# Optimization experiments

Measured on AMD Instinct MI355X. Metric: run time of the kernel, lower is better.

The kernel has to match this reference:

```python
import jax, jax.numpy as jnp
import numpy as np
import math

B, Q, CQ = 2, 2048, 512
H, D = 8, 64  # no_heads, c_hidden

def setup_inputs() -> dict:
    key = jax.random.key(0)
    ks = jax.random.split(key, 8)
    s = 0.02
    return {
        "q_x": jax.random.normal(ks[0], (B, Q, CQ), jnp.float32),
        "kv_x": jax.random.normal(ks[1], (B, Q, CQ), jnp.float32),
        "bias": jax.random.normal(ks[2], (B, 1, Q, Q), jnp.float32),
        "w_qkv": jax.random.normal(ks[3], (3 * H * D, CQ), jnp.float32) * s,
        "w_o": jax.random.normal(ks[4], (CQ, H * D), jnp.float32) * s,
        "b_o": jnp.zeros((CQ,), jnp.float32),
        "w_g": jax.random.normal(ks[5], (H * D, CQ), jnp.float32) * s,
        "b_g": jnp.zeros((H * D,), jnp.float32),
    }

def reference(q_x, kv_x, bias, w_qkv, w_o, b_o, w_g, b_g):
    # Fused QKV projection from q_x (kv_x is unused by the original module's _prep_qkv)
    qkv = jnp.einsum('bqc,ec->bqe', q_x, w_qkv)  # [B,Q,3*H*D]
    q, k, v = jnp.split(qkv, 3, axis=-1)
    q = q.reshape(B, Q, H, D) / math.sqrt(D)
    k = k.reshape(B, Q, H, D)
    v = v.reshape(B, Q, H, D)
    # scores + additive pairwise bias, softmax over keys
    scores = jnp.einsum('bqhd,bkhd->bhqk', q, k) + bias  # [B,H,Q,K]
    attn = jax.nn.softmax(scores, axis=-1)
    o = jnp.einsum('bhqk,bkhd->bqhd', attn, v)  # [B,Q,H,D]
    # sigmoid gating
    g = jax.nn.sigmoid(jnp.einsum('bqc,ec->bqe', q_x, w_g) + b_g).reshape(B, Q, H, D)
    o = o * g
    # output projection
    o = o.reshape(B, Q, H * D)
    return jnp.einsum('bqe,ce->bqc', o, w_o) + b_o
```

## Files before the change

kernel.cpp:

```cpp
#include <hip/hip_runtime.h>
#include <math.h>

#define B_  2
#define Q_  2048
#define CQ_ 512
#define H_  8
#define D_  64
#define M_  (B_*Q_)

typedef __bf16 bf16;
typedef __bf16 bf16x8 __attribute__((ext_vector_type(8)));
typedef float  f32x4  __attribute__((ext_vector_type(4)));

__device__ __forceinline__ void gl_lds16(const bf16* g, bf16* l) {
    __builtin_amdgcn_global_load_lds(
        (const __attribute__((address_space(1))) unsigned int*)g,
        (__attribute__((address_space(3))) unsigned int*)l, 16, 0, 0);
}

#define S0 (4096*512)
#define S1 (1536*512)
#define S2 (512*512)
#define S3 (512*512)
__global__ __launch_bounds__(256)
void convert_kernel(const float* __restrict__ qx, const float* __restrict__ wqkv,
                    const float* __restrict__ wg, const float* __restrict__ wo,
                    bf16* __restrict__ qxb, bf16* __restrict__ wcat, bf16* __restrict__ wob)
{
    const long long t = (long long)blockIdx.x * 256 + threadIdx.x;
    const long long e = t * 8;
    const float* src; bf16* dst;
    if (e < S0)                { src = qx + e;                  dst = qxb + e; }
    else if (e < S0 + S1)      { src = wqkv + (e - S0);         dst = wcat + (e - S0); }
    else if (e < S0 + S1 + S2) { src = wg + (e - S0 - S1);      dst = wcat + S1 + (e - S0 - S1); }
    else                       { src = wo + (e - S0 - S1 - S2); dst = wob + (e - S0 - S1 - S2); }
    const float4 a = *(const float4*)(src);
    const float4 b = *(const float4*)(src + 4);
    bf16x8 v;
    v[0] = (bf16)a.x; v[1] = (bf16)a.y; v[2] = (bf16)a.z; v[3] = (bf16)a.w;
    v[4] = (bf16)b.x; v[5] = (bf16)b.y; v[6] = (bf16)b.z; v[7] = (bf16)b.w;
    *(bf16x8*)dst = v;
}

template<int BM, int BN, int EPI>
__global__ __launch_bounds__(256)
void gemm_bf16(const bf16* __restrict__ A, const bf16* __restrict__ W,
               const float* __restrict__ bvec, float* __restrict__ fout,
               bf16* __restrict__ qb, bf16* __restrict__ kb, bf16* __restrict__ vb,
               bf16* __restrict__ gb)
{
    constexpr int MI = BM / 32, NJ = BN / 32;
    __shared__ __align__(16) bf16 As[BM * 32];
    __shared__ __align__(16) bf16 Bs[BN * 32];

    const int t = threadIdx.x;
    const int w = t >> 6, lane = t & 63;
    const int l15 = lane & 15, quad = lane >> 4;
    const int wm = w & 1, wn = w >> 1;
    const int bm = blockIdx.x * BM;
    const int bn = blockIdx.y * BN;

    f32x4 acc[MI][NJ] = {};

    const int rr = t >> 2;
    const int cc = (t & 3) * 8;

    for (int k0 = 0; k0 < 512; k0 += 32) {
        #pragma unroll
        for (int i = 0; i < BM / 64; ++i)
            gl_lds16(A + (size_t)(bm + i * 64 + rr) * 512 + k0 + cc,
                     As + (i * 64 + w * 16) * 32);
        #pragma unroll
        for (int i = 0; i < BN / 64; ++i)
            gl_lds16(W + (size_t)(bn + i * 64 + rr) * 512 + k0 + cc,
                     Bs + (i * 64 + w * 16) * 32);
        __asm__ volatile("s_waitcnt vmcnt(0)" ::: "memory");
        __syncthreads();

        bf16x8 af[MI], bfr[NJ];
        #pragma unroll
        for (int i = 0; i < MI; ++i)
            af[i] = *(const bf16x8*)(As + (wm * (BM / 2) + i * 16 + l15) * 32 + quad * 8);
        #pragma unroll
        for (int j = 0; j < NJ; ++j)
            bfr[j] = *(const bf16x8*)(Bs + (wn * (BN / 2) + j * 16 + l15) * 32 + quad * 8);
        #pragma unroll
        for (int i = 0; i < MI; ++i)
            #pragma unroll
            for (int j = 0; j < NJ; ++j)
                acc[i][j] = __builtin_amdgcn_mfma_f32_16x16x32_bf16(af[i], bfr[j], acc[i][j], 0, 0, 0);
        __syncthreads();
    }

    #pragma unroll
    for (int i = 0; i < MI; ++i) {
        #pragma unroll
        for (int r = 0; r < 4; ++r) {
            const int m = bm + wm * (BM / 2) + i * 16 + quad * 4 + r;
            const int b = m >> 11, qq = m & 2047;
            #pragma unroll
            for (int j = 0; j < NJ; ++j) {
                const int n = bn + wn * (BN / 2) + j * 16 + l15;
                const float c = acc[i][j][r];
                if constexpr (EPI == 0) {
                    const int part = n >> 9;
                    const int h = (n >> 6) & 7, d = n & 63;
                    if (part == 0)
                        qb[(((size_t)(b * H_ + h)) * Q_ + qq) * D_ + d] = (bf16)(c * 0.125f);
                    else if (part == 1)
                        kb[(((size_t)(b * H_ + h)) * Q_ + qq) * D_ + d] = (bf16)c;
                    else if (part == 2)
                        vb[(((size_t)(b * H_ + h)) * D_ + d) * Q_ + qq] = (bf16)c;
                    else {
                        const int gcol = n & 511;
                        const float x = c + bvec[gcol];
                        gb[(size_t)m * 512 + gcol] = (bf16)(1.f / (1.f + __expf(-x)));
                    }
                } else {
                    fout[(size_t)m * 512 + n] = c + bvec[n];
                }
            }
        }
    }
}

__global__ __launch_bounds__(256)
void attn_kernel(const bf16* __restrict__ qb, const bf16* __restrict__ kb,
                 const bf16* __restrict__ vb, const float* __restrict__ bias,
                 const bf16* __restrict__ g, bf16* __restrict__ og)
{
    __shared__ __align__(16) bf16 Ks[64 * 80];
    __shared__ __align__(16) bf16 Vs[64 * 80];
    __shared__ __align__(16) bf16 Ps[4][16 * 80];

    const int tid  = threadIdx.x;
    const int wv   = tid >> 6, lane = tid & 63;
    const int l15  = lane & 15, quad = lane >> 4;
    const int bh   = blockIdx.y;
    const int b    = bh >> 3, h = bh & 7;
    const int q0   = blockIdx.x * 64;
    const int qrow = q0 + wv * 16;

    const bf16* qptr = qb + ((size_t)bh * Q_ + qrow + l15) * D_;
    const bf16x8 aq0 = *(const bf16x8*)(qptr + quad * 8);
    const bf16x8 aq1 = *(const bf16x8*)(qptr + 32 + quad * 8);

    f32x4 acc_o[4] = {};
    float mrow[4] = {-INFINITY, -INFINITY, -INFINITY, -INFINITY};
    float lrow[4] = {0.f, 0.f, 0.f, 0.f};

    const bf16*  kbase = kb + (size_t)bh * Q_ * D_;
    const bf16*  vbase = vb + (size_t)bh * D_ * Q_;
    const float* brow  = bias + (size_t)b * Q_ * Q_;

    for (int k0 = 0; k0 < Q_; k0 += 64) {
        __syncthreads();
        #pragma unroll
        for (int p = 0; p < 2; ++p) {
            const int elem = p * 2048 + tid * 8;
            const int rr = elem >> 6, cc = elem & 63;
            *(float4*)(Ks + rr * 80 + cc) =
                *(const float4*)(kbase + (size_t)k0 * 64 + elem);
            *(float4*)(Vs + rr * 80 + cc) =
                *(const float4*)(vbase + (size_t)rr * Q_ + k0 + cc);
        }
        __syncthreads();

        float sc[4][4];
        #pragma unroll
        for (int kt = 0; kt < 4; ++kt) {
            f32x4 sacc = {0.f, 0.f, 0.f, 0.f};
            const bf16* kp = Ks + (kt * 16 + l15) * 80 + quad * 8;
            const bf16x8 bk0 = *(const bf16x8*)(kp);
            const bf16x8 bk1 = *(const bf16x8*)(kp + 32);
            sacc = __builtin_amdgcn_mfma_f32_16x16x32_bf16(aq0, bk0, sacc, 0, 0, 0);
            sacc = __builtin_amdgcn_mfma_f32_16x16x32_bf16(aq1, bk1, sacc, 0, 0, 0);
            const float* bp = brow + (size_t)(qrow + quad * 4) * Q_ + k0 + kt * 16 + l15;
            #pragma unroll
            for (int r = 0; r < 4; ++r) sc[kt][r] = sacc[r] + bp[(size_t)r * Q_];
        }

        float tmax[4];
        #pragma unroll
        for (int r = 0; r < 4; ++r)
            tmax[r] = fmaxf(fmaxf(sc[0][r], sc[1][r]), fmaxf(sc[2][r], sc[3][r]));
        #pragma unroll
        for (int off = 1; off < 16; off <<= 1)
            #pragma unroll
            for (int r = 0; r < 4; ++r)
                tmax[r] = fmaxf(tmax[r], __shfl_xor(tmax[r], off, 64));

        float alpha[4];
        #pragma unroll
        for (int r = 0; r < 4; ++r) {
            const float mn = fmaxf(mrow[r], tmax[r]);
            alpha[r] = __expf(mrow[r] - mn);
            mrow[r] = mn;
        }
        float rsum[4];
        #pragma unroll
        for (int r = 0; r < 4; ++r) {
            #pragma unroll
            for (int kt = 0; kt < 4; ++kt) sc[kt][r] = __expf(sc[kt][r] - mrow[r]);
            rsum[r] = sc[0][r] + sc[1][r] + sc[2][r] + sc[3][r];
        }
        #pragma unroll
        for (int off = 1; off < 16; off <<= 1)
            #pragma unroll
            for (int r = 0; r < 4; ++r)
                rsum[r] += __shfl_xor(rsum[r], off, 64);
        #pragma unroll
        for (int r = 0; r < 4; ++r) lrow[r] = lrow[r] * alpha[r] + rsum[r];
        #pragma unroll
        for (int dt = 0; dt < 4; ++dt)
            #pragma unroll
            for (int r = 0; r < 4; ++r) acc_o[dt][r] *= alpha[r];

        bf16* pw = Ps[wv];
        #pragma unroll
        for (int kt = 0; kt < 4; ++kt)
            #pragma unroll
            for (int r = 0; r < 4; ++r)
                pw[(quad * 4 + r) * 80 + kt * 16 + l15] = (bf16)sc[kt][r];
        __asm__ volatile("s_waitcnt lgkmcnt(0)" ::: "memory");

        #pragma unroll
        for (int kt2 = 0; kt2 < 2; ++kt2) {
            const bf16x8 ap = *(const bf16x8*)(pw + l15 * 80 + kt2 * 32 + quad * 8);
            #pragma unroll
            for (int dt = 0; dt < 4; ++dt) {
                const bf16x8 bv = *(const bf16x8*)(Vs + (dt * 16 + l15) * 80 + kt2 * 32 + quad * 8);
                acc_o[dt] = __builtin_amdgcn_mfma_f32_16x16x32_bf16(ap, bv, acc_o[dt], 0, 0, 0);
            }
        }
    }

    #pragma unroll
    for (int r = 0; r < 4; ++r) {
        const float inv = 1.f / lrow[r];
        const int qg = qrow + quad * 4 + r;
        const size_t rowoff = ((size_t)(b * Q_ + qg)) * 512 + h * 64;
        #pragma unroll
        for (int dt = 0; dt < 4; ++dt) {
            const int col = dt * 16 + l15;
            og[rowoff + col] = (bf16)(acc_o[dt][r] * inv * (float)g[rowoff + col]);
        }
    }
}

extern "C" void kernel_launch(void* const* d_in, const int* in_sizes, int n_in,
                              void* d_out, int out_size, void* d_ws, size_t ws_size,
                              hipStream_t stream)
{
    const float* q_x   = (const float*)d_in[0];
    const float* bias  = (const float*)d_in[2];
    const float* w_qkv = (const float*)d_in[3];
    const float* w_o   = (const float*)d_in[4];
    const float* b_o   = (const float*)d_in[5];
    const float* w_g   = (const float*)d_in[6];
    const float* b_g   = (const float*)d_in[7];
    float* out = (float*)d_out;

    char* ws = (char*)d_ws;
    bf16* qxb  = (bf16*)(ws);
    bf16* wcat = (bf16*)(ws + (4u  << 20));
    bf16* wob  = (bf16*)(ws + (6u  << 20));
    bf16* qb   = (bf16*)(ws + (8u  << 20));
    bf16* kb   = (bf16*)(ws + (12u << 20));
    bf16* vb   = (bf16*)(ws + (16u << 20));
    bf16* gb   = (bf16*)(ws + (20u << 20));
    bf16* ogb  = (bf16*)(ws + (24u << 20));

    convert_kernel<<<(S0 + S1 + S2 + S3) / (256 * 8), 256, 0, stream>>>(
        q_x, w_qkv, w_g, w_o, qxb, wcat, wob);
    gemm_bf16<128, 128, 0><<<dim3(32, 16), 256, 0, stream>>>(
        qxb, wcat, b_g, nullptr, qb, kb, vb, gb);
    attn_kernel<<<dim3(Q_ / 64, B_ * H_), 256, 0, stream>>>(qb, kb, vb, bias, gb, ogb);
    gemm_bf16<64, 128, 1><<<dim3(64, 4), 256, 0, stream>>>(
        ogb, wob, b_o, out, nullptr, nullptr, nullptr, nullptr);
}
```

Baseline: 204.2 us.

## Double-buffer K/V tiles, transpose MFMA operands, vectorize bias loads in attention

Restructures the attention kernel to compute S^T (K as the A operand, Q as B), so each lane owns one query row. Bias can then be loaded as contiguous float4 and the softmax reductions need only two cross-lane shuffles instead of four per value. K/V tiles and bias are prefetched into registers one iteration ahead into a double-buffered LDS with padding 72, which removes one barrier per iteration. The grid is also reordered so that the blocks of one query tile, which share bias rows across heads, run close together. The cost is higher register pressure from the prefetch buffers and more LDS use.

```diff
diff --git a/kernel.cpp b/kernel.cpp
--- a/kernel.cpp
+++ b/kernel.cpp
@@ -9,6 +9,7 @@
 #define M_  (B_*Q_)
 
 typedef __bf16 bf16;
+typedef __bf16 bf16x4 __attribute__((ext_vector_type(4)));
 typedef __bf16 bf16x8 __attribute__((ext_vector_type(8)));
 typedef float  f32x4  __attribute__((ext_vector_type(4)));
 
@@ -129,122 +130,147 @@
                  const bf16* __restrict__ vb, const float* __restrict__ bias,
                  const bf16* __restrict__ g, bf16* __restrict__ og)
 {
-    __shared__ __align__(16) bf16 Ks[64 * 80];
-    __shared__ __align__(16) bf16 Vs[64 * 80];
-    __shared__ __align__(16) bf16 Ps[4][16 * 80];
+    __shared__ __align__(16) bf16 Ks[2][64 * 72];
+    __shared__ __align__(16) bf16 Vs[2][64 * 72];
+    __shared__ __align__(16) bf16 Ps[4][16 * 72];
 
     const int tid  = threadIdx.x;
     const int wv   = tid >> 6, lane = tid & 63;
     const int l15  = lane & 15, quad = lane >> 4;
-    const int bh   = blockIdx.y;
+    const int bh   = blockIdx.x;
     const int b    = bh >> 3, h = bh & 7;
-    const int q0   = blockIdx.x * 64;
-    const int qrow = q0 + wv * 16;
-
-    const bf16* qptr = qb + ((size_t)bh * Q_ + qrow + l15) * D_;
-    const bf16x8 aq0 = *(const bf16x8*)(qptr + quad * 8);
-    const bf16x8 aq1 = *(const bf16x8*)(qptr + 32 + quad * 8);
-
-    f32x4 acc_o[4] = {};
-    float mrow[4] = {-INFINITY, -INFINITY, -INFINITY, -INFINITY};
-    float lrow[4] = {0.f, 0.f, 0.f, 0.f};
+    const int q0   = blockIdx.y * 64;
+    const int qrow = q0 + wv * 16 + l15;
+
+    const bf16* qptr = qb + ((size_t)bh * Q_ + qrow) * D_;
+    const bf16x8 bq0 = *(const bf16x8*)(qptr + quad * 8);
+    const bf16x8 bq1 = *(const bf16x8*)(qptr + 32 + quad * 8);
+
+    f32x4 acc[4] = {};
+    float m_run = -INFINITY, l_run = 0.f;
 
     const bf16*  kbase = kb + (size_t)bh * Q_ * D_;
     const bf16*  vbase = vb + (size_t)bh * D_ * Q_;
-    const float* brow  = bias + (size_t)b * Q_ * Q_;
-
-    for (int k0 = 0; k0 < Q_; k0 += 64) {
-        __syncthreads();
-        #pragma unroll
-        for (int p = 0; p < 2; ++p) {
-            const int elem = p * 2048 + tid * 8;
-            const int rr = elem >> 6, cc = elem & 63;
-            *(float4*)(Ks + rr * 80 + cc) =
-                *(const float4*)(kbase + (size_t)k0 * 64 + elem);
-            *(float4*)(Vs + rr * 80 + cc) =
-                *(const float4*)(vbase + (size_t)rr * Q_ + k0 + cc);
-        }
-        __syncthreads();
+    const float* brow  = bias + ((size_t)b * Q_ + qrow) * Q_;
+
+    const int sr  = tid >> 3;
+    const int sc8 = (tid & 7) * 8;
+
+    float4 kreg0, kreg1, vreg0, vreg1;
+    float4 bias_cur[4], bias_nxt[4];
+
+    kreg0 = *(const float4*)(kbase + (size_t)sr * 64 + sc8);
+    kreg1 = *(const float4*)(kbase + (size_t)(32 + sr) * 64 + sc8);
+    vreg0 = *(const float4*)(vbase + (size_t)sr * Q_ + sc8);
+    vreg1 = *(const float4*)(vbase + (size_t)(32 + sr) * Q_ + sc8);
+    #pragma unroll
+    for (int kt = 0; kt < 4; ++kt)
+        bias_cur[kt] = *(const float4*)(brow + kt * 16 + quad * 4);
+    *(float4*)(Ks[0] + sr * 72 + sc8) = kreg0;
+    *(float4*)(Ks[0] + (32 + sr) * 72 + sc8) = kreg1;
+    *(float4*)(Vs[0] + sr * 72 + sc8) = vreg0;
+    *(float4*)(Vs[0] + (32 + sr) * 72 + sc8) = vreg1;
+    __syncthreads();
+
+    int cur = 0;
+    for (int t = 0; t < 32; ++t) {
+        if (t < 31) {
+            const int k0n = (t + 1) * 64;
+            kreg0 = *(const float4*)(kbase + ((size_t)k0n + sr) * 64 + sc8);
+            kreg1 = *(const float4*)(kbase + ((size_t)k0n + 32 + sr) * 64 + sc8);
+            vreg0 = *(const float4*)(vbase + (size_t)sr * Q_ + k0n + sc8);
+            vreg1 = *(const float4*)(vbase + (size_t)(32 + sr) * Q_ + k0n + sc8);
+            #pragma unroll
+            for (int kt = 0; kt < 4; ++kt)
+                bias_nxt[kt] = *(const float4*)(brow + k0n + kt * 16 + quad * 4);
+        }
+
+        const bf16* Kc = Ks[cur];
+        const bf16* Vc = Vs[cur];
 
         float sc[4][4];
         #pragma unroll
         for (int kt = 0; kt < 4; ++kt) {
             f32x4 sacc = {0.f, 0.f, 0.f, 0.f};
-            const bf16* kp = Ks + (kt * 16 + l15) * 80 + quad * 8;
-            const bf16x8 bk0 = *(const bf16x8*)(kp);
-            const bf16x8 bk1 = *(const bf16x8*)(kp + 32);
-            sacc = __builtin_amdgcn_mfma_f32_16x16x32_bf16(aq0, bk0, sacc, 0, 0, 0);
-            sacc = __builtin_amdgcn_mfma_f32_16x16x32_bf16(aq1, bk1, sacc, 0, 0, 0);
-            const float* bp = brow + (size_t)(qrow + quad * 4) * Q_ + k0 + kt * 16 + l15;
-            #pragma unroll
-            for (int r = 0; r < 4; ++r) sc[kt][r] = sacc[r] + bp[(size_t)r * Q_];
-        }
-
-        float tmax[4];
+            const bf16* kp = Kc + (kt * 16 + l15) * 72 + quad * 8;
+            const bf16x8 ak0 = *(const bf16x8*)(kp);
+            const bf16x8 ak1 = *(const bf16x8*)(kp + 32);
+            sacc = __builtin_amdgcn_mfma_f32_16x16x32_bf16(ak0, bq0, sacc, 0, 0, 0);
+            sacc = __builtin_amdgcn_mfma_f32_16x16x32_bf16(ak1, bq1, sacc, 0, 0, 0);
+            sc[kt][0] = sacc[0] + bias_cur[kt].x;
+            sc[kt][1] = sacc[1] + bias_cur[kt].y;
+            sc[kt][2] = sacc[2] + bias_cur[kt].z;
+            sc[kt][3] = sacc[3] + bias_cur[kt].w;
+        }
+
+        float tmax = -INFINITY;
+        #pragma unroll
+        for (int kt = 0; kt < 4; ++kt)
+            tmax = fmaxf(tmax, fmaxf(fmaxf(sc[kt][0], sc[kt][1]),
+                                     fmaxf(sc[kt][2], sc[kt][3])));
+        tmax = fmaxf(tmax, __shfl_xor(tmax, 16, 64));
+        tmax = fmaxf(tmax, __shfl_xor(tmax, 32, 64));
+
+        const float mn = fmaxf(m_run, tmax);
+        const float alpha = __expf(m_run - mn);
+        m_run = mn;
+
+        float rsum = 0.f;
+        #pragma unroll
+        for (int kt = 0; kt < 4; ++kt)
+            #pragma unroll
+            for (int r = 0; r < 4; ++r) {
+                sc[kt][r] = __expf(sc[kt][r] - mn);
+                rsum += sc[kt][r];
+            }
+        rsum += __shfl_xor(rsum, 16, 64);
+        rsum += __shfl_xor(rsum, 32, 64);
+        l_run = l_run * alpha + rsum;
+        #pragma unroll
+        for (int dt = 0; dt < 4; ++dt) acc[dt] *= alpha;
+
+        bf16* pw = Ps[wv] + l15 * 72;
+        #pragma unroll
+        for (int kt = 0; kt < 4; ++kt) {
+            bf16x4 p4;
+            p4[0] = (bf16)sc[kt][0]; p4[1] = (bf16)sc[kt][1];
+            p4[2] = (bf16)sc[kt][2]; p4[3] = (bf16)sc[kt][3];
+            *(bf16x4*)(pw + kt * 16 + quad * 4) = p4;
+        }
+        __asm__ volatile("s_waitcnt lgkmcnt(0)" ::: "memory");
+
+        #pragma unroll
+        for (int kt2 = 0; kt2 < 2; ++kt2) {
+            const bf16x8 bp = *(const bf16x8*)(pw + kt2 * 32 + quad * 8);
+            #pragma unroll
+            for (int dt = 0; dt < 4; ++dt) {
+                const bf16x8 av = *(const bf16x8*)(Vc + (dt * 16 + l15) * 72 + kt2 * 32 + quad * 8);
+                acc[dt] = __builtin_amdgcn_mfma_f32_16x16x32_bf16(av, bp, acc[dt], 0, 0, 0);
+            }
+        }
+
+        if (t < 31) {
+            *(float4*)(Ks[cur ^ 1] + sr * 72 + sc8) = kreg0;
+            *(float4*)(Ks[cur ^ 1] + (32 + sr) * 72 + sc8) = kreg1;
+            *(float4*)(Vs[cur ^ 1] + sr * 72 + sc8) = vreg0;
+            *(float4*)(Vs[cur ^ 1] + (32 + sr) * 72 + sc8) = vreg1;
+            #pragma unroll
+            for (int kt = 0; kt < 4; ++kt) bias_cur[kt] = bias_nxt[kt];
+        }
+        __syncthreads();
+        cur ^= 1;
+    }
+
+    const float inv = 1.f / l_run;
+    const size_t obase = ((size_t)(b * Q_ + qrow)) * 512 + h * 64;
+    #pragma unroll
+    for (int dt = 0; dt < 4; ++dt) {
+        const bf16x4 gv = *(const bf16x4*)(g + obase + dt * 16 + quad * 4);
+        bf16x4 ov;
         #pragma unroll
         for (int r = 0; r < 4; ++r)
-            tmax[r] = fmaxf(fmaxf(sc[0][r], sc[1][r]), fmaxf(sc[2][r], sc[3][r]));
-        #pragma unroll
-        for (int off = 1; off < 16; off <<= 1)
-            #pragma unroll
-            for (int r = 0; r < 4; ++r)
-                tmax[r] = fmaxf(tmax[r], __shfl_xor(tmax[r], off, 64));
-
-        float alpha[4];
-        #pragma unroll
-        for (int r = 0; r < 4; ++r) {
-            const float mn = fmaxf(mrow[r], tmax[r]);
-            alpha[r] = __expf(mrow[r] - mn);
-            mrow[r] = mn;
-        }
-        float rsum[4];
-        #pragma unroll
-        for (int r = 0; r < 4; ++r) {
-            #pragma unroll
-            for (int kt = 0; kt < 4; ++kt) sc[kt][r] = __expf(sc[kt][r] - mrow[r]);
-            rsum[r] = sc[0][r] + sc[1][r] + sc[2][r] + sc[3][r];
-        }
-        #pragma unroll
-        for (int off = 1; off < 16; off <<= 1)
-            #pragma unroll
-            for (int r = 0; r < 4; ++r)
-                rsum[r] += __shfl_xor(rsum[r], off, 64);
-        #pragma unroll
-        for (int r = 0; r < 4; ++r) lrow[r] = lrow[r] * alpha[r] + rsum[r];
-        #pragma unroll
-        for (int dt = 0; dt < 4; ++dt)
-            #pragma unroll
-            for (int r = 0; r < 4; ++r) acc_o[dt][r] *= alpha[r];
-
-        bf16* pw = Ps[wv];
-        #pragma unroll
-        for (int kt = 0; kt < 4; ++kt)
-            #pragma unroll
-            for (int r = 0; r < 4; ++r)
-                pw[(quad * 4 + r) * 80 + kt * 16 + l15] = (bf16)sc[kt][r];
-        __asm__ volatile("s_waitcnt lgkmcnt(0)" ::: "memory");
-
-        #pragma unroll
-        for (int kt2 = 0; kt2 < 2; ++kt2) {
-            const bf16x8 ap = *(const bf16x8*)(pw + l15 * 80 + kt2 * 32 + quad * 8);
-            #pragma unroll
-            for (int dt = 0; dt < 4; ++dt) {
-                const bf16x8 bv = *(const bf16x8*)(Vs + (dt * 16 + l15) * 80 + kt2 * 32 + quad * 8);
-                acc_o[dt] = __builtin_amdgcn_mfma_f32_16x16x32_bf16(ap, bv, acc_o[dt], 0, 0, 0);
-            }
-        }
-    }
-
-    #pragma unroll
-    for (int r = 0; r < 4; ++r) {
-        const float inv = 1.f / lrow[r];
-        const int qg = qrow + quad * 4 + r;
-        const size_t rowoff = ((size_t)(b * Q_ + qg)) * 512 + h * 64;
-        #pragma unroll
-        for (int dt = 0; dt < 4; ++dt) {
-            const int col = dt * 16 + l15;
-            og[rowoff + col] = (bf16)(acc_o[dt][r] * inv * (float)g[rowoff + col]);
-        }
+            ov[r] = (bf16)(acc[dt][r] * inv * (float)gv[r]);
+        *(bf16x4*)(og + obase + dt * 16 + quad * 4) = ov;
     }
 }
 
@@ -275,7 +301,7 @@
         q_x, w_qkv, w_g, w_o, qxb, wcat, wob);
     gemm_bf16<128, 128, 0><<<dim3(32, 16), 256, 0, stream>>>(
         qxb, wcat, b_g, nullptr, qb, kb, vb, gb);
-    attn_kernel<<<dim3(Q_ / 64, B_ * H_), 256, 0, stream>>>(qb, kb, vb, bias, gb, ogb);
+    attn_kernel<<<dim3(B_ * H_, Q_ / 64), 256, 0, stream>>>(qb, kb, vb, bias, gb, ogb);
     gemm_bf16<64, 128, 1><<<dim3(64, 4), 256, 0, stream>>>(
         ogb, wob, b_o, out, nullptr, nullptr, nullptr, nullptr);
 }
```

Result: faster. 180.8 us (-11.5%).
